# Performance work log

Measured on AMD Instinct MI355X. Metric: run time of the kernel, lower is better.

## Reference

```python
import jax, jax.numpy as jnp
import numpy as np

HIDDEN = 1024
B, S = 4, 2048

def setup_inputs() -> dict:
    key = jax.random.key(0)
    ks = jax.random.split(key, 8)
    scale = 1.0 / np.sqrt(HIDDEN)
    return {
        "x": jax.random.normal(ks[0], (B, S, HIDDEN), dtype=jnp.float32),
        "mask": jax.random.randint(ks[1], (B, S, S), 0, 2, dtype=jnp.int32),
        "Wq": jax.random.normal(ks[2], (HIDDEN, HIDDEN), dtype=jnp.float32) * scale,
        "bq": jax.random.normal(ks[3], (HIDDEN,), dtype=jnp.float32) * 0.01,
        "Wk": jax.random.normal(ks[4], (HIDDEN, HIDDEN), dtype=jnp.float32) * scale,
        "bk": jax.random.normal(ks[5], (HIDDEN,), dtype=jnp.float32) * 0.01,
        "Wv": jax.random.normal(ks[6], (HIDDEN, HIDDEN), dtype=jnp.float32) * scale,
        "bv": jax.random.normal(ks[7], (HIDDEN,), dtype=jnp.float32) * 0.01,
    }

def reference(x, mask, Wq, bq, Wk, bk, Wv, bv):
    # torch Linear: y = x @ W.T + b
    Q = jnp.einsum("bsh,oh->bso", x, Wq) + bq
    K = jnp.einsum("bsh,oh->bso", x, Wk) + bk
    V = jnp.einsum("bsh,oh->bso", x, Wv) + bv
    inv_sqrt_h = 1.0 / jnp.sqrt(jnp.asarray(Q.shape[-1], Q.dtype))
    score = jnp.einsum("bqh,bkh->bqk", Q, K) * inv_sqrt_h  # [B, S, S]
    score = jnp.where(mask == 0, jnp.asarray(-jnp.inf, score.dtype), score)
    attn = jax.nn.softmax(score, axis=-1)
    return jnp.einsum("bqk,bkh->bqh", attn, V)
```

## Files before the change

### kernel.cpp

```cpp
#include <hip/hip_runtime.h>

using u16 = unsigned short;
using u32 = unsigned int;

typedef __attribute__((ext_vector_type(4))) float f32x4;
typedef __attribute__((ext_vector_type(8))) short s16x8;

__device__ __forceinline__ u16 f2b(float f) {
  u32 u = __builtin_bit_cast(u32, f);
  u += 0x7FFFu + ((u >> 16) & 1u);
  return (u16)(u >> 16);
}
__device__ __forceinline__ float b2f(u16 h) {
  return __builtin_bit_cast(float, (u32)h << 16);
}
__device__ __forceinline__ void gl_lds16(const void* g, void* l) {
  __builtin_amdgcn_global_load_lds(
      (const __attribute__((address_space(1))) void*)g,
      (__attribute__((address_space(3))) void*)l, 16, 0, 0);
}
template<int N> __device__ __forceinline__ void waitvm() {
  static_assert(N == 4 || N == 3 || N == 0, "literal");
  if constexpr (N == 4)      asm volatile("s_waitcnt vmcnt(4)" ::: "memory");
  else if constexpr (N == 3) asm volatile("s_waitcnt vmcnt(3)" ::: "memory");
  else                       asm volatile("s_waitcnt vmcnt(0)" ::: "memory");
}
__device__ __forceinline__ void barrier_np() {
  __builtin_amdgcn_s_barrier();
  asm volatile("" ::: "memory");
}

__global__ __launch_bounds__(256) void convert4_k(
    const float* __restrict__ x, const float* __restrict__ Wq,
    const float* __restrict__ Wk, const float* __restrict__ Wv,
    u16* __restrict__ dst) {
  long g = (long)(blockIdx.x * 256 + threadIdx.x) * 8;
  const float* s;
  if (g < 8388608L)       s = x  + g;
  else if (g < 9437184L)  s = Wq + (g - 8388608L);
  else if (g < 10485760L) s = Wk + (g - 9437184L);
  else                    s = Wv + (g - 10485760L);
  f32x4 lo = *(const f32x4*)s;
  f32x4 hi = *(const f32x4*)(s + 4);
  s16x8 o;
  #pragma unroll
  for (int e = 0; e < 4; ++e) { o[e] = (short)f2b(lo[e]); o[4 + e] = (short)f2b(hi[e]); }
  *(s16x8*)(dst + g) = o;
}

template<int EPI, int NWC>
__global__ __launch_bounds__(128 * NWC, 2) void gemm_nt(
    const u16* __restrict__ A, const u16* __restrict__ B0,
    const u16* __restrict__ W2, const u16* __restrict__ W3,
    int lda, int ldb, int K, long za, long zb, long ze,
    const float* __restrict__ bq, const float* __restrict__ bk, const float* __restrict__ bv,
    u16* __restrict__ qw, u16* __restrict__ kw, u16* __restrict__ vt,
    const int* __restrict__ mask, u16* __restrict__ sc, float* __restrict__ outO)
{
  constexpr int THREADS = 128 * NWC;
  constexpr int LOGW    = (NWC == 2) ? 1 : 2;
  constexpr int BN      = 64 * NWC;
  constexpr int ACH     = 512;
  constexpr int CH      = ACH + BN * 4;
  constexpr int CALLS   = CH / THREADS;
  constexpr int SLOT    = CH * 8;
  __shared__ __align__(16) u16 lds[3 * SLOT];

  const int tid  = threadIdx.x;
  const int wave = tid >> 6, lane = tid & 63;
  const int wr = wave >> LOGW, wc = wave & (NWC - 1);
  const int m0 = blockIdx.y * 128, n0 = blockIdx.x * BN;
  const long z = blockIdx.z;
  A += z * za;

  const u16* Bsrc = B0;
  int nbase = n0;
  if constexpr (EPI == 0) {
    Bsrc = (n0 < 1024) ? B0 : (n0 < 2048) ? W2 : W3;
    nbase = n0 & 1023;
  }
  Bsrc += z * zb;

  const u16* gsrc[CALLS];
  u32 loff[CALLS];
  #pragma unroll
  for (int c = 0; c < CALLS; ++c) {
    int qq  = c * THREADS + tid;
    int isB = qq >= ACH;
    int r   = (isB ? qq - ACH : qq) >> 2;
    int kc  = (qq & 3) ^ ((r >> 1) & 3);
    gsrc[c] = (isB ? (Bsrc + (size_t)(nbase + r) * ldb)
                   : (A    + (size_t)(m0    + r) * lda)) + kc * 8;
    loff[c] = (u32)qq * 8;
  }

  const int frow = lane & 15;
  const int q    = lane >> 4;
  u32 aoff[4], boff[4];
  #pragma unroll
  for (int i = 0; i < 4; ++i) {
    int lr = wr * 64 + i * 16 + frow;
    aoff[i] = (u32)lr * 32 + (u32)((q ^ ((lr >> 1) & 3)) << 3);
  }
  #pragma unroll
  for (int j = 0; j < 4; ++j) {
    int lc = wc * 64 + j * 16 + frow;
    boff[j] = (u32)ACH * 8 + (u32)lc * 32 + (u32)((q ^ ((lc >> 1) & 3)) << 3);
  }

  f32x4 acc[4][4];
  const f32x4 fz = {0.f, 0.f, 0.f, 0.f};
  #pragma unroll
  for (int i = 0; i < 4; ++i)
    #pragma unroll
    for (int j = 0; j < 4; ++j) acc[i][j] = fz;

  const int NT = K >> 5;

  auto tile_compute = [&](const u16* buf) {
    s16x8 bf[4], af[4];
    #pragma unroll
    for (int j = 0; j < 4; ++j) bf[j] = *(const s16x8*)(buf + boff[j]);
    #pragma unroll
    for (int i = 0; i < 4; ++i) af[i] = *(const s16x8*)(buf + aoff[i]);
    __builtin_amdgcn_s_setprio(1);
    #pragma unroll
    for (int i = 0; i < 4; ++i)
      #pragma unroll
      for (int j = 0; j < 4; ++j)
        acc[i][j] = __builtin_amdgcn_mfma_f32_16x16x32_bf16(af[i], bf[j], acc[i][j], 0, 0, 0);
    __builtin_amdgcn_s_setprio(0);
  };

  #pragma unroll
  for (int c = 0; c < CALLS; ++c) gl_lds16(gsrc[c],      lds        + loff[c]);
  #pragma unroll
  for (int c = 0; c < CALLS; ++c) gl_lds16(gsrc[c] + 32, lds + SLOT + loff[c]);

  int rd = 0, st = 2;
  for (int T = 0; T < NT - 2; ++T) {
    waitvm<CALLS>();
    barrier_np();
    u16* sb = lds + (size_t)st * SLOT;
    const size_t koff = (size_t)(T + 2) * 32;
    #pragma unroll
    for (int c = 0; c < CALLS; ++c) gl_lds16(gsrc[c] + koff, sb + loff[c]);
    tile_compute(lds + (size_t)rd * SLOT);
    rd = (rd == 2) ? 0 : rd + 1;
    st = (st == 2) ? 0 : st + 1;
  }
  waitvm<CALLS>(); barrier_np(); tile_compute(lds + (size_t)rd * SLOT);
  rd = (rd == 2) ? 0 : rd + 1;
  waitvm<0>();     barrier_np(); tile_compute(lds + (size_t)rd * SLOT);

  const int r0 = (lane >> 4) * 4;
  const int ccol = lane & 15;
  #pragma unroll
  for (int i = 0; i < 4; ++i) {
    #pragma unroll
    for (int j = 0; j < 4; ++j) {
      #pragma unroll
      for (int r = 0; r < 4; ++r) {
        int R = m0 + wr * 64 + i * 16 + r0 + r;
        int C = n0 + wc * 64 + j * 16 + ccol;
        float v = acc[i][j][r];
        if constexpr (EPI == 0) {
          int sec = C >> 10, nl = C & 1023;
          v += (sec == 0) ? bq[nl] : (sec == 1) ? bk[nl] : bv[nl];
          u16 o = f2b(v);
          int b = R >> 11, s = R & 2047;
          if (sec == 0)      qw[(size_t)R * 1024 + nl] = o;
          else if (sec == 1) kw[(size_t)R * 1024 + nl] = o;
          else               vt[(size_t)b * 2097152u + (size_t)nl * 2048 + s] = o;
        } else if constexpr (EPI == 1) {
          v *= 0.03125f;
          size_t idx = (size_t)(z * ze) + (size_t)R * 2048 + C;
          if (mask[idx] == 0) v = -__builtin_inff();
          sc[idx] = f2b(v);
        } else {
          outO[(size_t)(z * ze) + (size_t)R * 1024 + C] = v;
        }
      }
    }
  }
}

__global__ __launch_bounds__(256) void softmax_k(u16* __restrict__ Sc) {
  __shared__ float red[8];
  u16* p = Sc + (size_t)blockIdx.x * 2048;
  const int tid = threadIdx.x;
  const int lane = tid & 63, wv = tid >> 6;
  s16x8 u = *(const s16x8*)(p + tid * 8);
  float v[8];
  #pragma unroll
  for (int e = 0; e < 8; ++e) v[e] = b2f((u16)u[e]);
  float mx = v[0];
  #pragma unroll
  for (int e = 1; e < 8; ++e) mx = fmaxf(mx, v[e]);
  #pragma unroll
  for (int off = 32; off > 0; off >>= 1) mx = fmaxf(mx, __shfl_xor(mx, off));
  if (lane == 0) red[wv] = mx;
  __syncthreads();
  mx = fmaxf(fmaxf(red[0], red[1]), fmaxf(red[2], red[3]));
  float s = 0.f;
  #pragma unroll
  for (int e = 0; e < 8; ++e) { v[e] = __expf(v[e] - mx); s += v[e]; }
  #pragma unroll
  for (int off = 32; off > 0; off >>= 1) s += __shfl_xor(s, off);
  if (lane == 0) red[4 + wv] = s;
  __syncthreads();
  s = (red[4] + red[5]) + (red[6] + red[7]);
  float inv = 1.f / s;
  s16x8 o;
  #pragma unroll
  for (int e = 0; e < 8; ++e) o[e] = (short)f2b(v[e] * inv);
  *(s16x8*)(p + tid * 8) = o;
}

extern "C" void kernel_launch(void* const* d_in, const int* in_sizes, int n_in,
                              void* d_out, int out_size, void* d_ws, size_t ws_size,
                              hipStream_t stream) {
  const float* x  = (const float*)d_in[0];
  const int* mask = (const int*)d_in[1];
  const float* Wq = (const float*)d_in[2];
  const float* bq = (const float*)d_in[3];
  const float* Wk = (const float*)d_in[4];
  const float* bk = (const float*)d_in[5];
  const float* Wv = (const float*)d_in[6];
  const float* bv = (const float*)d_in[7];
  float* out = (float*)d_out;
  char* ws = (char*)d_ws;

  u16* xc  = (u16*)ws;
  u16* Wqc = (u16*)(ws + (16u << 20));
  u16* Wkc = (u16*)(ws + (18u << 20));
  u16* Wvc = (u16*)(ws + (20u << 20));
  u16* Qw  = (u16*)(ws + (22u << 20));
  u16* Kw  = (u16*)(ws + (38u << 20));
  u16* Vt  = (u16*)(ws + (54u << 20));
  u16* Sc  = (u16*)(ws + (70u << 20));

  convert4_k<<<5632, 256, 0, stream>>>(x, Wq, Wk, Wv, xc);

  gemm_nt<0, 2><<<dim3(24, 64, 1), 256, 0, stream>>>(
      xc, Wqc, Wkc, Wvc, 1024, 1024, 1024, 0, 0, 0,
      bq, bk, bv, Qw, Kw, Vt, nullptr, nullptr, nullptr);
  gemm_nt<1, 4><<<dim3(8, 16, 4), 512, 0, stream>>>(
      Qw, Kw, nullptr, nullptr, 1024, 1024, 1024, 2097152, 2097152, 4194304,
      nullptr, nullptr, nullptr, nullptr, nullptr, nullptr, mask, Sc, nullptr);
  softmax_k<<<8192, 256, 0, stream>>>(Sc);
  gemm_nt<2, 2><<<dim3(8, 16, 4), 256, 0, stream>>>(
      Sc, Vt, nullptr, nullptr, 2048, 2048, 2048, 4194304, 2097152, 2097152,
      nullptr, nullptr, nullptr, nullptr, nullptr, nullptr, nullptr, nullptr, out);
}
```

Baseline: 331.7 us.

## Deepen GEMM pipeline to 4 LDS stages with register double-buffered fragments

Moves the shared GEMM kernel from a 3-stage to a 4-stage LDS ring with three tiles prefetched, and double-buffers the MFMA operand fragments in registers so the LDS reads for the next tile overlap the current tile's MFMAs. It also drops the 512-thread NWC=4 variant, so the QK^T score GEMM now runs as 256-thread 128x128 tiles on a grid twice as wide. This aims to hide global-load and LDS-read latency, at the cost of more LDS per block and more registers, which could lower occupancy.

```diff
diff --git a/kernel.cpp b/kernel.cpp
--- a/kernel.cpp
+++ b/kernel.cpp
@@ -20,9 +20,9 @@
       (__attribute__((address_space(3))) void*)l, 16, 0, 0);
 }
 template<int N> __device__ __forceinline__ void waitvm() {
-  static_assert(N == 4 || N == 3 || N == 0, "literal");
-  if constexpr (N == 4)      asm volatile("s_waitcnt vmcnt(4)" ::: "memory");
-  else if constexpr (N == 3) asm volatile("s_waitcnt vmcnt(3)" ::: "memory");
+  static_assert(N == 8 || N == 4 || N == 0, "literal");
+  if constexpr (N == 8)      asm volatile("s_waitcnt vmcnt(8)" ::: "memory");
+  else if constexpr (N == 4) asm volatile("s_waitcnt vmcnt(4)" ::: "memory");
   else                       asm volatile("s_waitcnt vmcnt(0)" ::: "memory");
 }
 __device__ __forceinline__ void barrier_np() {
@@ -48,8 +48,8 @@
   *(s16x8*)(dst + g) = o;
 }
 
-template<int EPI, int NWC>
-__global__ __launch_bounds__(128 * NWC, 2) void gemm_nt(
+template<int EPI>
+__global__ __launch_bounds__(256, 2) void gemm_nt(
     const u16* __restrict__ A, const u16* __restrict__ B0,
     const u16* __restrict__ W2, const u16* __restrict__ W3,
     int lda, int ldb, int K, long za, long zb, long ze,
@@ -57,19 +57,16 @@
     u16* __restrict__ qw, u16* __restrict__ kw, u16* __restrict__ vt,
     const int* __restrict__ mask, u16* __restrict__ sc, float* __restrict__ outO)
 {
-  constexpr int THREADS = 128 * NWC;
-  constexpr int LOGW    = (NWC == 2) ? 1 : 2;
-  constexpr int BN      = 64 * NWC;
-  constexpr int ACH     = 512;
-  constexpr int CH      = ACH + BN * 4;
-  constexpr int CALLS   = CH / THREADS;
-  constexpr int SLOT    = CH * 8;
-  __shared__ __align__(16) u16 lds[3 * SLOT];
+  constexpr int ACH   = 512;
+  constexpr int CH    = 1024;
+  constexpr int CALLS = 4;
+  constexpr int SLOT  = CH * 8;
+  __shared__ __align__(16) u16 lds[4 * SLOT];
 
   const int tid  = threadIdx.x;
   const int wave = tid >> 6, lane = tid & 63;
-  const int wr = wave >> LOGW, wc = wave & (NWC - 1);
-  const int m0 = blockIdx.y * 128, n0 = blockIdx.x * BN;
+  const int wr = wave >> 1, wc = wave & 1;
+  const int m0 = blockIdx.y * 128, n0 = blockIdx.x * 128;
   const long z = blockIdx.z;
   A += z * za;
 
@@ -85,7 +82,7 @@
   u32 loff[CALLS];
   #pragma unroll
   for (int c = 0; c < CALLS; ++c) {
-    int qq  = c * THREADS + tid;
+    int qq  = c * 256 + tid;
     int isB = qq >= ACH;
     int r   = (isB ? qq - ACH : qq) >> 2;
     int kc  = (qq & 3) ^ ((r >> 1) & 3);
@@ -117,41 +114,50 @@
 
   const int NT = K >> 5;
 
-  auto tile_compute = [&](const u16* buf) {
-    s16x8 bf[4], af[4];
-    #pragma unroll
-    for (int j = 0; j < 4; ++j) bf[j] = *(const s16x8*)(buf + boff[j]);
-    #pragma unroll
-    for (int i = 0; i < 4; ++i) af[i] = *(const s16x8*)(buf + aoff[i]);
+  auto body = [&](int T, s16x8 (&ca)[4], s16x8 (&cb)[4],
+                  s16x8 (&na)[4], s16x8 (&nb)[4], bool stg, bool rd) {
+    if (T < NT - 2) waitvm<CALLS>(); else waitvm<0>();
+    barrier_np();
+    if (stg) {
+      u16* sb = lds + (size_t)((T + 3) & 3) * SLOT;
+      const size_t koff = (size_t)(T + 3) * 32;
+      #pragma unroll
+      for (int c = 0; c < CALLS; ++c) gl_lds16(gsrc[c] + koff, sb + loff[c]);
+    }
+    if (rd) {
+      const u16* nbuf = lds + (size_t)((T + 1) & 3) * SLOT;
+      #pragma unroll
+      for (int j = 0; j < 4; ++j) nb[j] = *(const s16x8*)(nbuf + boff[j]);
+      #pragma unroll
+      for (int i = 0; i < 4; ++i) na[i] = *(const s16x8*)(nbuf + aoff[i]);
+    }
     __builtin_amdgcn_s_setprio(1);
     #pragma unroll
     for (int i = 0; i < 4; ++i)
       #pragma unroll
       for (int j = 0; j < 4; ++j)
-        acc[i][j] = __builtin_amdgcn_mfma_f32_16x16x32_bf16(af[i], bf[j], acc[i][j], 0, 0, 0);
+        acc[i][j] = __builtin_amdgcn_mfma_f32_16x16x32_bf16(ca[i], cb[j], acc[i][j], 0, 0, 0);
     __builtin_amdgcn_s_setprio(0);
   };
 
   #pragma unroll
-  for (int c = 0; c < CALLS; ++c) gl_lds16(gsrc[c],      lds        + loff[c]);
-  #pragma unroll
-  for (int c = 0; c < CALLS; ++c) gl_lds16(gsrc[c] + 32, lds + SLOT + loff[c]);
-
-  int rd = 0, st = 2;
-  for (int T = 0; T < NT - 2; ++T) {
-    waitvm<CALLS>();
-    barrier_np();
-    u16* sb = lds + (size_t)st * SLOT;
-    const size_t koff = (size_t)(T + 2) * 32;
-    #pragma unroll
-    for (int c = 0; c < CALLS; ++c) gl_lds16(gsrc[c] + koff, sb + loff[c]);
-    tile_compute(lds + (size_t)rd * SLOT);
-    rd = (rd == 2) ? 0 : rd + 1;
-    st = (st == 2) ? 0 : st + 1;
-  }
-  waitvm<CALLS>(); barrier_np(); tile_compute(lds + (size_t)rd * SLOT);
-  rd = (rd == 2) ? 0 : rd + 1;
-  waitvm<0>();     barrier_np(); tile_compute(lds + (size_t)rd * SLOT);
+  for (int c = 0; c < CALLS; ++c) gl_lds16(gsrc[c],      lds            + loff[c]);
+  #pragma unroll
+  for (int c = 0; c < CALLS; ++c) gl_lds16(gsrc[c] + 32, lds + SLOT     + loff[c]);
+  #pragma unroll
+  for (int c = 0; c < CALLS; ++c) gl_lds16(gsrc[c] + 64, lds + 2 * SLOT + loff[c]);
+  waitvm<8>();
+  barrier_np();
+  s16x8 fa[4], fb[4], ga[4], gb[4];
+  #pragma unroll
+  for (int j = 0; j < 4; ++j) fb[j] = *(const s16x8*)(lds + boff[j]);
+  #pragma unroll
+  for (int i = 0; i < 4; ++i) fa[i] = *(const s16x8*)(lds + aoff[i]);
+
+  for (int T = 0; T < NT; T += 2) {
+    body(T,     fa, fb, ga, gb, T     < NT - 3, true);
+    body(T + 1, ga, gb, fa, fb, T + 1 < NT - 3, T + 2 < NT);
+  }
 
   const int r0 = (lane >> 4) * 4;
   const int ccol = lane & 15;
@@ -242,14 +248,14 @@
 
   convert4_k<<<5632, 256, 0, stream>>>(x, Wq, Wk, Wv, xc);
 
-  gemm_nt<0, 2><<<dim3(24, 64, 1), 256, 0, stream>>>(
+  gemm_nt<0><<<dim3(24, 64, 1), 256, 0, stream>>>(
       xc, Wqc, Wkc, Wvc, 1024, 1024, 1024, 0, 0, 0,
       bq, bk, bv, Qw, Kw, Vt, nullptr, nullptr, nullptr);
-  gemm_nt<1, 4><<<dim3(8, 16, 4), 512, 0, stream>>>(
+  gemm_nt<1><<<dim3(16, 16, 4), 256, 0, stream>>>(
       Qw, Kw, nullptr, nullptr, 1024, 1024, 1024, 2097152, 2097152, 4194304,
       nullptr, nullptr, nullptr, nullptr, nullptr, nullptr, mask, Sc, nullptr);
   softmax_k<<<8192, 256, 0, stream>>>(Sc);
-  gemm_nt<2, 2><<<dim3(8, 16, 4), 256, 0, stream>>>(
+  gemm_nt<2><<<dim3(8, 16, 4), 256, 0, stream>>>(
       Sc, Vt, nullptr, nullptr, 2048, 2048, 2048, 4194304, 2097152, 2097152,
       nullptr, nullptr, nullptr, nullptr, nullptr, nullptr, nullptr, nullptr, out);
 }
```

New measurement: 343.0 us. 3.4% more time.
